# Kernel tuning notes

Measured on AMD Instinct MI355X. Metric: run time of the kernel, lower is better.

Reference implementation:

```python
import jax, jax.numpy as jnp
import numpy as np

D = 128  # input_dim

def setup_inputs() -> dict:
    key = jax.random.key(0)
    ks = jax.random.split(key, 9)
    B, Lq, Lkv = 4, 4096, 4096
    s = 1.0 / np.sqrt(D)
    return {
        "x1": jax.random.normal(ks[0], (B, Lq, D), dtype=jnp.float32),
        "x2": jax.random.normal(ks[1], (B, Lkv, D), dtype=jnp.float32),
        "x3": jax.random.normal(ks[2], (B, Lkv, D), dtype=jnp.float32),
        "Wq": jax.random.normal(ks[3], (D, D), dtype=jnp.float32) * s,
        "bq": jax.random.normal(ks[4], (D,), dtype=jnp.float32) * s,
        "Wk": jax.random.normal(ks[5], (D, D), dtype=jnp.float32) * s,
        "bk": jax.random.normal(ks[6], (D,), dtype=jnp.float32) * s,
        "Wv": jax.random.normal(ks[7], (D, D), dtype=jnp.float32) * s,
        "bv": jax.random.normal(ks[8], (D,), dtype=jnp.float32) * s,
    }

def reference(x1, x2, x3, Wq, bq, Wk, bk, Wv, bv):
    # torch Linear: y = x @ W.T + b
    q = jnp.einsum('bld,ed->ble', x1, Wq) + bq  # [B,Lq,D]
    k = jnp.einsum('bld,ed->ble', x2, Wk) + bk  # [B,Lkv,D]
    v = jnp.einsum('bld,ed->ble', x3, Wv) + bv  # [B,Lkv,D]
    scores = jnp.einsum('bqd,bkd->bqk', q, k) / jnp.sqrt(jnp.float32(x1.shape[-1]))
    attn = jax.nn.softmax(scores, axis=2)
    return jnp.einsum('bqk,bkd->bqd', attn, v)
```

## Files before the change

kernel.cpp:

```cpp
#include <hip/hip_runtime.h>
#include <hip/hip_bf16.h>

typedef __attribute__((ext_vector_type(8))) short short8;
typedef __attribute__((ext_vector_type(4))) float v4f;

__device__ __forceinline__ unsigned short f2bf(float f) {
    union { float f; unsigned u; } c; c.f = f;
    unsigned r = c.u + 0x7FFFu + ((c.u >> 16) & 1u);
    return (unsigned short)(r >> 16);
}
__device__ __forceinline__ unsigned pack2(float a, float b) {
    return (unsigned)f2bf(a) | ((unsigned)f2bf(b) << 16);
}

__device__ __forceinline__ void g2l16(const unsigned short* g, unsigned short* l) {
    __builtin_amdgcn_global_load_lds(
        (const __attribute__((address_space(1))) unsigned int*)g,
        (__attribute__((address_space(3))) unsigned int*)l,
        16, 0, 0);
}

__global__ __launch_bounds__(512) void proj_kernel(
    const float* __restrict__ x1, const float* __restrict__ x2, const float* __restrict__ x3,
    const float* __restrict__ Wq, const float* __restrict__ bq,
    const float* __restrict__ Wk, const float* __restrict__ bk,
    const float* __restrict__ Wv, const float* __restrict__ bv,
    unsigned short* __restrict__ qb, unsigned short* __restrict__ kb,
    unsigned short* __restrict__ vb, float qscale)
{
    __shared__ __attribute__((aligned(16))) unsigned short Xs[16384];
    __shared__ __attribute__((aligned(16))) unsigned short Ws[16384];

    int tid = threadIdx.x;
    int wave = tid >> 6, lane = tid & 63;
    int lmod = lane & 15, ldiv = lane >> 4;
    int p = blockIdx.x % 3;
    int row0 = (blockIdx.x / 3) * 128;

    const float* X = p == 0 ? x1 : p == 1 ? x2 : x3;
    const float* W = p == 0 ? Wq : p == 1 ? Wk : Wv;
    const float* bias = p == 0 ? bq : p == 1 ? bk : bv;
    float scale = p == 0 ? qscale : 1.0f;

#pragma unroll
    for (int i = 0; i < 8; i++) {
        int c = tid + i * 512;
        int row = c >> 5, d0 = (c & 31) * 4;
        v4f f = *(const v4f*)(X + (size_t)(row0 + row) * 128 + d0);
        int off = ((row >> 4) * 16 + (d0 >> 5) * 4 + ((d0 >> 3) & 3)) * 128 + (row & 15) * 8 + (d0 & 7);
        *(uint2*)&Xs[off] = make_uint2(pack2(f[0], f[1]), pack2(f[2], f[3]));
        v4f g = *(const v4f*)(W + (size_t)row * 128 + d0);
        *(uint2*)&Ws[off] = make_uint2(pack2(g[0], g[1]), pack2(g[2], g[3]));
    }
    __syncthreads();

    short8 af[4];
#pragma unroll
    for (int kc = 0; kc < 4; kc++)
        af[kc] = *(const short8*)&Xs[wave * 2048 + (kc * 4 + ldiv) * 128 + lmod * 8];

#pragma unroll
    for (int ct = 0; ct < 8; ct++) {
        v4f acc = {0.f, 0.f, 0.f, 0.f};
#pragma unroll
        for (int kc = 0; kc < 4; kc++) {
            short8 bf = *(const short8*)&Ws[ct * 2048 + (kc * 4 + ldiv) * 128 + lmod * 8];
            acc = __builtin_amdgcn_mfma_f32_16x16x32_bf16(af[kc], bf, acc, 0, 0, 0);
        }
        int e = ct * 16 + lmod;
        float bv_ = bias[e];
#pragma unroll
        for (int r = 0; r < 4; r++) {
            int orow = row0 + wave * 16 + ldiv * 4 + r;
            unsigned short h = f2bf((acc[r] + bv_) * scale);
            if (p == 0) {
                qb[(size_t)orow * 128 + e] = h;
            } else if (p == 1) {
                int b = orow >> 12, key = orow & 4095;
                kb[b * 524288 + (key >> 4) * 2048 + ((e >> 5) * 4 + ((e >> 3) & 3)) * 128 + (key & 15) * 8 + (e & 7)] = h;
            } else {
                int b = orow >> 12, key = orow & 4095;
                vb[b * 524288 + (key >> 5) * 4096 + ((e >> 4) * 4 + ((key >> 3) & 3)) * 128 + (e & 15) * 8 + (key & 7)] = h;
            }
        }
    }
}

__global__ __launch_bounds__(512, 2) void attn_kernel(
    const unsigned short* __restrict__ Qb,
    const unsigned short* __restrict__ Kb,
    const unsigned short* __restrict__ Vb,
    float* __restrict__ Out)
{
    __shared__ __attribute__((aligned(16))) unsigned short Kt[2][2][8192];
    __shared__ __attribute__((aligned(16))) unsigned short Vt[2][2][8192];
    __shared__ __attribute__((aligned(16))) unsigned short Ps[8][1088];

    int tid = threadIdx.x;
    int wave = tid >> 6, lane = tid & 63;
    int lmod = lane & 15, ldiv = lane >> 4;
    int g = wave >> 2, wq = wave & 3;
    int b = blockIdx.x & 3, qblk = blockIdx.x >> 2;
    int q0 = qblk * 64 + wq * 16;

    const unsigned short* qptr = Qb + (size_t)(b * 4096 + q0 + lmod) * 128;
    short8 qfrag[4];
#pragma unroll
    for (int kc = 0; kc < 4; kc++)
        qfrag[kc] = *(const short8*)(qptr + kc * 32 + ldiv * 8);

    v4f oacc[8];
#pragma unroll
    for (int dt = 0; dt < 8; dt++) oacc[dt] = (v4f){0.f, 0.f, 0.f, 0.f};
    float lsum[4] = {0.f, 0.f, 0.f, 0.f};

    const unsigned short* kbase = Kb + b * 524288 + g * 262144;
    const unsigned short* vbase = Vb + b * 524288 + g * 262144;

#pragma unroll
    for (int i = 0; i < 4; i++) {
        g2l16(kbase + wq * 2048 + i * 512 + lane * 8, &Kt[g][0][wq * 2048 + i * 512]);
        g2l16(vbase + wq * 2048 + i * 512 + lane * 8, &Vt[g][0][wq * 2048 + i * 512]);
    }
    __syncthreads();

    for (int t = 0; t < 32; t++) {
        int cur = t & 1;
        if (t < 31) {
            const unsigned short* kg = kbase + (t + 1) * 8192;
            const unsigned short* vg = vbase + (t + 1) * 8192;
#pragma unroll
            for (int i = 0; i < 4; i++) {
                g2l16(kg + wq * 2048 + i * 512 + lane * 8, &Kt[g][cur ^ 1][wq * 2048 + i * 512]);
                g2l16(vg + wq * 2048 + i * 512 + lane * 8, &Vt[g][cur ^ 1][wq * 2048 + i * 512]);
            }
        }

        v4f sacc[4];
#pragma unroll
        for (int s = 0; s < 4; s++) {
            sacc[s] = (v4f){0.f, 0.f, 0.f, 0.f};
#pragma unroll
            for (int kc = 0; kc < 4; kc++) {
                short8 kf = *(const short8*)&Kt[g][cur][s * 2048 + (kc * 4 + ldiv) * 128 + lmod * 8];
                sacc[s] = __builtin_amdgcn_mfma_f32_16x16x32_bf16(qfrag[kc], kf, sacc[s], 0, 0, 0);
            }
        }

#pragma unroll
        for (int r = 0; r < 4; r++) {
            float p0 = __builtin_amdgcn_exp2f(sacc[0][r]);
            float p1 = __builtin_amdgcn_exp2f(sacc[1][r]);
            float p2 = __builtin_amdgcn_exp2f(sacc[2][r]);
            float p3 = __builtin_amdgcn_exp2f(sacc[3][r]);
            lsum[r] += (p0 + p1) + (p2 + p3);
            int ro = (ldiv * 4 + r) * 68 + lmod;
            Ps[wave][ro]      = f2bf(p0);
            Ps[wave][ro + 16] = f2bf(p1);
            Ps[wave][ro + 32] = f2bf(p2);
            Ps[wave][ro + 48] = f2bf(p3);
        }
        asm volatile("s_waitcnt lgkmcnt(0)" ::: "memory");

        short8 pf0 = *(const short8*)&Ps[wave][lmod * 68 + ldiv * 8];
        short8 pf1 = *(const short8*)&Ps[wave][lmod * 68 + 32 + ldiv * 8];
#pragma unroll
        for (int dt = 0; dt < 8; dt++) {
            short8 vf0 = *(const short8*)&Vt[g][cur][(dt * 4 + ldiv) * 128 + lmod * 8];
            short8 vf1 = *(const short8*)&Vt[g][cur][4096 + (dt * 4 + ldiv) * 128 + lmod * 8];
            oacc[dt] = __builtin_amdgcn_mfma_f32_16x16x32_bf16(pf0, vf0, oacc[dt], 0, 0, 0);
            oacc[dt] = __builtin_amdgcn_mfma_f32_16x16x32_bf16(pf1, vf1, oacc[dt], 0, 0, 0);
        }
        __syncthreads();
    }

#pragma unroll
    for (int r = 0; r < 4; r++) {
        lsum[r] += __shfl_xor(lsum[r], 1);
        lsum[r] += __shfl_xor(lsum[r], 2);
        lsum[r] += __shfl_xor(lsum[r], 4);
        lsum[r] += __shfl_xor(lsum[r], 8);
    }

    float* Obuf = (float*)&Kt[0][0][0];
    float* Ml   = (float*)&Vt[0][0][0];
    if (g == 1) {
#pragma unroll
        for (int r = 0; r < 4; r++) {
            int row = ldiv * 4 + r;
#pragma unroll
            for (int dt = 0; dt < 8; dt++)
                Obuf[(wq * 16 + row) * 128 + dt * 16 + lmod] = oacc[dt][r];
            if (lmod == 0) Ml[wq * 16 + row] = lsum[r];
        }
    }
    __syncthreads();
    if (g == 0) {
        float* obase = Out + (size_t)(b * 4096 + q0) * 128;
#pragma unroll
        for (int r = 0; r < 4; r++) {
            int row = ldiv * 4 + r;
            float inv = 1.0f / (lsum[r] + Ml[wq * 16 + row]);
#pragma unroll
            for (int dt = 0; dt < 8; dt++) {
                float v = (oacc[dt][r] + Obuf[(wq * 16 + row) * 128 + dt * 16 + lmod]) * inv;
                obase[(size_t)row * 128 + dt * 16 + lmod] = v;
            }
        }
    }
}

extern "C" void kernel_launch(void* const* d_in, const int* in_sizes, int n_in,
                              void* d_out, int out_size, void* d_ws, size_t ws_size,
                              hipStream_t stream) {
    const float* x1 = (const float*)d_in[0];
    const float* x2 = (const float*)d_in[1];
    const float* x3 = (const float*)d_in[2];
    const float* Wq = (const float*)d_in[3];
    const float* bq = (const float*)d_in[4];
    const float* Wk = (const float*)d_in[5];
    const float* bk = (const float*)d_in[6];
    const float* Wv = (const float*)d_in[7];
    const float* bv = (const float*)d_in[8];
    float* out = (float*)d_out;

    unsigned short* qb = (unsigned short*)d_ws;
    unsigned short* kb = qb + (size_t)16384 * 128;
    unsigned short* vb = kb + (size_t)16384 * 128;

    const float qscale = 1.4426950408889634f / 11.313708498984761f;

    proj_kernel<<<384, 512, 0, stream>>>(x1, x2, x3, Wq, bq, Wk, bk, Wv, bv,
                                         qb, kb, vb, qscale);
    attn_kernel<<<256, 512, 0, stream>>>(qb, kb, vb, out);
}
```

Before: 161.3 us.

## Split KV across blocks with bf16 partial outputs and a separate merge kernel

```diff
diff --git a/kernel.cpp b/kernel.cpp
--- a/kernel.cpp
+++ b/kernel.cpp
@@ -11,6 +11,10 @@
 }
 __device__ __forceinline__ unsigned pack2(float a, float b) {
     return (unsigned)f2bf(a) | ((unsigned)f2bf(b) << 16);
+}
+__device__ __forceinline__ float bf2f(unsigned short h) {
+    union { unsigned u; float f; } c; c.u = ((unsigned)h) << 16;
+    return c.f;
 }
 
 __device__ __forceinline__ void g2l16(const unsigned short* g, unsigned short* l) {
@@ -76,137 +80,152 @@
             if (p == 0) {
                 qb[(size_t)orow * 128 + e] = h;
             } else if (p == 1) {
-                int b = orow >> 12, key = orow & 4095;
-                kb[b * 524288 + (key >> 4) * 2048 + ((e >> 5) * 4 + ((e >> 3) & 3)) * 128 + (key & 15) * 8 + (e & 7)] = h;
+                int b = orow >> 12, key = orow & 4095, kk = key & 31;
+                kb[b * 524288 + (key >> 5) * 4096 + (kk & 1) * 2048
+                   + ((e >> 5) * 4 + ((e >> 3) & 3)) * 128 + (kk >> 1) * 8 + (e & 7)] = h;
             } else {
                 int b = orow >> 12, key = orow & 4095;
-                vb[b * 524288 + (key >> 5) * 4096 + ((e >> 4) * 4 + ((key >> 3) & 3)) * 128 + (e & 15) * 8 + (key & 7)] = h;
+                vb[b * 524288 + (key >> 5) * 4096
+                   + ((e >> 4) * 4 + ((key >> 3) & 3)) * 128 + (e & 15) * 8 + (key & 7)] = h;
             }
         }
     }
 }
 
-__global__ __launch_bounds__(512, 2) void attn_kernel(
+__global__ __launch_bounds__(256, 2) void attn_kernel(
     const unsigned short* __restrict__ Qb,
     const unsigned short* __restrict__ Kb,
     const unsigned short* __restrict__ Vb,
-    float* __restrict__ Out)
+    unsigned short* __restrict__ Opart,
+    float* __restrict__ Lbuf)
 {
-    __shared__ __attribute__((aligned(16))) unsigned short Kt[2][2][8192];
-    __shared__ __attribute__((aligned(16))) unsigned short Vt[2][2][8192];
-    __shared__ __attribute__((aligned(16))) unsigned short Ps[8][1088];
+    __shared__ __attribute__((aligned(16))) unsigned short Kt[2][4096];
+    __shared__ __attribute__((aligned(16))) unsigned short Vt[2][4096];
+    __shared__ __attribute__((aligned(16))) unsigned short Ps[4][1280];
 
     int tid = threadIdx.x;
     int wave = tid >> 6, lane = tid & 63;
     int lmod = lane & 15, ldiv = lane >> 4;
-    int g = wave >> 2, wq = wave & 3;
-    int b = blockIdx.x & 3, qblk = blockIdx.x >> 2;
-    int q0 = qblk * 64 + wq * 16;
-
-    const unsigned short* qptr = Qb + (size_t)(b * 4096 + q0 + lmod) * 128;
-    short8 qfrag[4];
-#pragma unroll
-    for (int kc = 0; kc < 4; kc++)
-        qfrag[kc] = *(const short8*)(qptr + kc * 32 + ldiv * 8);
-
-    v4f oacc[8];
-#pragma unroll
-    for (int dt = 0; dt < 8; dt++) oacc[dt] = (v4f){0.f, 0.f, 0.f, 0.f};
-    float lsum[4] = {0.f, 0.f, 0.f, 0.f};
-
-    const unsigned short* kbase = Kb + b * 524288 + g * 262144;
-    const unsigned short* vbase = Vb + b * 524288 + g * 262144;
-
-#pragma unroll
-    for (int i = 0; i < 4; i++) {
-        g2l16(kbase + wq * 2048 + i * 512 + lane * 8, &Kt[g][0][wq * 2048 + i * 512]);
-        g2l16(vbase + wq * 2048 + i * 512 + lane * 8, &Vt[g][0][wq * 2048 + i * 512]);
+    int split = blockIdx.x & 3;
+    int qidx = blockIdx.x >> 2;
+    int b = qidx >> 5;
+    int q0 = (qidx & 31) * 128 + wave * 32;
+
+    short8 qfrag[2][4];
+#pragma unroll
+    for (int set = 0; set < 2; set++) {
+        const unsigned short* qptr = Qb + (size_t)(b * 4096 + q0 + set * 16 + lmod) * 128;
+#pragma unroll
+        for (int kc = 0; kc < 4; kc++)
+            qfrag[set][kc] = *(const short8*)(qptr + kc * 32 + ldiv * 8);
+    }
+
+    v4f oacc[2][8];
+#pragma unroll
+    for (int set = 0; set < 2; set++)
+#pragma unroll
+        for (int dt = 0; dt < 8; dt++) oacc[set][dt] = (v4f){0.f, 0.f, 0.f, 0.f};
+    float lsum[2][4] = {{0.f, 0.f, 0.f, 0.f}, {0.f, 0.f, 0.f, 0.f}};
+
+    const unsigned short* kbase = Kb + b * 524288 + split * 131072;
+    const unsigned short* vbase = Vb + b * 524288 + split * 131072;
+
+#pragma unroll
+    for (int i = 0; i < 2; i++) {
+        g2l16(kbase + wave * 1024 + i * 512 + lane * 8, &Kt[0][wave * 1024 + i * 512]);
+        g2l16(vbase + wave * 1024 + i * 512 + lane * 8, &Vt[0][wave * 1024 + i * 512]);
     }
     __syncthreads();
 
     for (int t = 0; t < 32; t++) {
         int cur = t & 1;
         if (t < 31) {
-            const unsigned short* kg = kbase + (t + 1) * 8192;
-            const unsigned short* vg = vbase + (t + 1) * 8192;
-#pragma unroll
-            for (int i = 0; i < 4; i++) {
-                g2l16(kg + wq * 2048 + i * 512 + lane * 8, &Kt[g][cur ^ 1][wq * 2048 + i * 512]);
-                g2l16(vg + wq * 2048 + i * 512 + lane * 8, &Vt[g][cur ^ 1][wq * 2048 + i * 512]);
+            const unsigned short* kg = kbase + (t + 1) * 4096;
+            const unsigned short* vg = vbase + (t + 1) * 4096;
+#pragma unroll
+            for (int i = 0; i < 2; i++) {
+                g2l16(kg + wave * 1024 + i * 512 + lane * 8, &Kt[cur ^ 1][wave * 1024 + i * 512]);
+                g2l16(vg + wave * 1024 + i * 512 + lane * 8, &Vt[cur ^ 1][wave * 1024 + i * 512]);
             }
         }
 
-        v4f sacc[4];
+        v4f sacc[2][2];
+#pragma unroll
+        for (int set = 0; set < 2; set++)
+#pragma unroll
+            for (int s = 0; s < 2; s++) sacc[set][s] = (v4f){0.f, 0.f, 0.f, 0.f};
+#pragma unroll
+        for (int kc = 0; kc < 4; kc++) {
+            short8 kf0 = *(const short8*)&Kt[cur][(kc * 4 + ldiv) * 128 + lmod * 8];
+            short8 kf1 = *(const short8*)&Kt[cur][2048 + (kc * 4 + ldiv) * 128 + lmod * 8];
+            sacc[0][0] = __builtin_amdgcn_mfma_f32_16x16x32_bf16(qfrag[0][kc], kf0, sacc[0][0], 0, 0, 0);
+            sacc[0][1] = __builtin_amdgcn_mfma_f32_16x16x32_bf16(qfrag[0][kc], kf1, sacc[0][1], 0, 0, 0);
+            sacc[1][0] = __builtin_amdgcn_mfma_f32_16x16x32_bf16(qfrag[1][kc], kf0, sacc[1][0], 0, 0, 0);
+            sacc[1][1] = __builtin_amdgcn_mfma_f32_16x16x32_bf16(qfrag[1][kc], kf1, sacc[1][1], 0, 0, 0);
+        }
+
+#pragma unroll
+        for (int set = 0; set < 2; set++)
+#pragma unroll
+            for (int r = 0; r < 4; r++) {
+                float p0 = __builtin_amdgcn_exp2f(sacc[set][0][r]);
+                float p1 = __builtin_amdgcn_exp2f(sacc[set][1][r]);
+                lsum[set][r] += p0 + p1;
+                *(unsigned*)&Ps[wave][(set * 16 + 4 * ldiv + r) * 40 + lmod * 2] = pack2(p0, p1);
+            }
+        asm volatile("s_waitcnt lgkmcnt(0)" ::: "memory");
+
+        short8 pf0 = *(const short8*)&Ps[wave][lmod * 40 + ldiv * 8];
+        short8 pf1 = *(const short8*)&Ps[wave][(16 + lmod) * 40 + ldiv * 8];
+#pragma unroll
+        for (int dt = 0; dt < 8; dt++) {
+            short8 vf = *(const short8*)&Vt[cur][(dt * 4 + ldiv) * 128 + lmod * 8];
+            oacc[0][dt] = __builtin_amdgcn_mfma_f32_16x16x32_bf16(pf0, vf, oacc[0][dt], 0, 0, 0);
+            oacc[1][dt] = __builtin_amdgcn_mfma_f32_16x16x32_bf16(pf1, vf, oacc[1][dt], 0, 0, 0);
+        }
+        __syncthreads();
+    }
+
+#pragma unroll
+    for (int set = 0; set < 2; set++)
+#pragma unroll
+        for (int r = 0; r < 4; r++) {
+            float lv = lsum[set][r];
+            lv += __shfl_xor(lv, 1);
+            lv += __shfl_xor(lv, 2);
+            lv += __shfl_xor(lv, 4);
+            lv += __shfl_xor(lv, 8);
+            int gq = b * 4096 + q0 + set * 16 + 4 * ldiv + r;
+            if (lmod == 0) Lbuf[split * 16384 + gq] = lv;
+            unsigned short* obase = Opart + (size_t)(split * 16384 + gq) * 128;
+#pragma unroll
+            for (int dt = 0; dt < 8; dt++)
+                obase[dt * 16 + lmod] = f2bf(oacc[set][dt][r]);
+        }
+}
+
+__global__ __launch_bounds__(256) void merge_kernel(
+    const unsigned short* __restrict__ Opart,
+    const float* __restrict__ Lbuf,
+    float* __restrict__ Out)
+{
+    int t = blockIdx.x * 256 + threadIdx.x;
+#pragma unroll
+    for (int it = 0; it < 4; it++) {
+        int base = (t + it * 65536) * 8;
+        int q = base >> 7;
+        float inv = 1.0f / (Lbuf[q] + Lbuf[16384 + q] + Lbuf[32768 + q] + Lbuf[49152 + q]);
+        float acc[8] = {0.f, 0.f, 0.f, 0.f, 0.f, 0.f, 0.f, 0.f};
 #pragma unroll
         for (int s = 0; s < 4; s++) {
-            sacc[s] = (v4f){0.f, 0.f, 0.f, 0.f};
-#pragma unroll
-            for (int kc = 0; kc < 4; kc++) {
-                short8 kf = *(const short8*)&Kt[g][cur][s * 2048 + (kc * 4 + ldiv) * 128 + lmod * 8];
-                sacc[s] = __builtin_amdgcn_mfma_f32_16x16x32_bf16(qfrag[kc], kf, sacc[s], 0, 0, 0);
-            }
-        }
-
-#pragma unroll
-        for (int r = 0; r < 4; r++) {
-            float p0 = __builtin_amdgcn_exp2f(sacc[0][r]);
-            float p1 = __builtin_amdgcn_exp2f(sacc[1][r]);
-            float p2 = __builtin_amdgcn_exp2f(sacc[2][r]);
-            float p3 = __builtin_amdgcn_exp2f(sacc[3][r]);
-            lsum[r] += (p0 + p1) + (p2 + p3);
-            int ro = (ldiv * 4 + r) * 68 + lmod;
-            Ps[wave][ro]      = f2bf(p0);
-            Ps[wave][ro + 16] = f2bf(p1);
-            Ps[wave][ro + 32] = f2bf(p2);
-            Ps[wave][ro + 48] = f2bf(p3);
-        }
-        asm volatile("s_waitcnt lgkmcnt(0)" ::: "memory");
-
-        short8 pf0 = *(const short8*)&Ps[wave][lmod * 68 + ldiv * 8];
-        short8 pf1 = *(const short8*)&Ps[wave][lmod * 68 + 32 + ldiv * 8];
-#pragma unroll
-        for (int dt = 0; dt < 8; dt++) {
-            short8 vf0 = *(const short8*)&Vt[g][cur][(dt * 4 + ldiv) * 128 + lmod * 8];
-            short8 vf1 = *(const short8*)&Vt[g][cur][4096 + (dt * 4 + ldiv) * 128 + lmod * 8];
-            oacc[dt] = __builtin_amdgcn_mfma_f32_16x16x32_bf16(pf0, vf0, oacc[dt], 0, 0, 0);
-            oacc[dt] = __builtin_amdgcn_mfma_f32_16x16x32_bf16(pf1, vf1, oacc[dt], 0, 0, 0);
-        }
-        __syncthreads();
-    }
-
-#pragma unroll
-    for (int r = 0; r < 4; r++) {
-        lsum[r] += __shfl_xor(lsum[r], 1);
-        lsum[r] += __shfl_xor(lsum[r], 2);
-        lsum[r] += __shfl_xor(lsum[r], 4);
-        lsum[r] += __shfl_xor(lsum[r], 8);
-    }
-
-    float* Obuf = (float*)&Kt[0][0][0];
-    float* Ml   = (float*)&Vt[0][0][0];
-    if (g == 1) {
-#pragma unroll
-        for (int r = 0; r < 4; r++) {
-            int row = ldiv * 4 + r;
-#pragma unroll
-            for (int dt = 0; dt < 8; dt++)
-                Obuf[(wq * 16 + row) * 128 + dt * 16 + lmod] = oacc[dt][r];
-            if (lmod == 0) Ml[wq * 16 + row] = lsum[r];
-        }
-    }
-    __syncthreads();
-    if (g == 0) {
-        float* obase = Out + (size_t)(b * 4096 + q0) * 128;
-#pragma unroll
-        for (int r = 0; r < 4; r++) {
-            int row = ldiv * 4 + r;
-            float inv = 1.0f / (lsum[r] + Ml[wq * 16 + row]);
-#pragma unroll
-            for (int dt = 0; dt < 8; dt++) {
-                float v = (oacc[dt][r] + Obuf[(wq * 16 + row) * 128 + dt * 16 + lmod]) * inv;
-                obase[(size_t)row * 128 + dt * 16 + lmod] = v;
-            }
-        }
+            short8 o = *(const short8*)(Opart + (size_t)s * 2097152 + base);
+#pragma unroll
+            for (int j = 0; j < 8; j++) acc[j] += bf2f((unsigned short)o[j]);
+        }
+        v4f lo = {acc[0] * inv, acc[1] * inv, acc[2] * inv, acc[3] * inv};
+        v4f hi = {acc[4] * inv, acc[5] * inv, acc[6] * inv, acc[7] * inv};
+        *(v4f*)(Out + base) = lo;
+        *(v4f*)(Out + base + 4) = hi;
     }
 }
 
@@ -225,12 +244,15 @@
     float* out = (float*)d_out;
 
     unsigned short* qb = (unsigned short*)d_ws;
-    unsigned short* kb = qb + (size_t)16384 * 128;
-    unsigned short* vb = kb + (size_t)16384 * 128;
+    unsigned short* kb = qb + (size_t)2097152;
+    unsigned short* vb = kb + (size_t)2097152;
+    unsigned short* op = vb + (size_t)2097152;
+    float* lb = (float*)(op + (size_t)8388608);
 
     const float qscale = 1.4426950408889634f / 11.313708498984761f;
 
     proj_kernel<<<384, 512, 0, stream>>>(x1, x2, x3, Wq, bq, Wk, bk, Wv, bv,
                                          qb, kb, vb, qscale);
-    attn_kernel<<<256, 512, 0, stream>>>(qb, kb, vb, out);
-}
+    attn_kernel<<<512, 256, 0, stream>>>(qb, kb, vb, op, lb);
+    merge_kernel<<<256, 256, 0, stream>>>(op, lb, out);
+}
```

Result: faster. 140.8 us (-12.7%).
